# Optimization experiments

Measured on AMD Instinct MI355X. Metric: run time of the kernel, lower is better.

The kernel has to match this reference:

```python
import jax, jax.numpy as jnp
import numpy as np

VOCAB = 32000
D = 256
B, S = 16, 128


def setup_inputs() -> dict:
    key = jax.random.key(0)
    ks = jax.random.split(key, 8)
    s = 1.0 / np.sqrt(D)
    return {
        "X": jax.random.randint(ks[0], (B, S), 0, VOCAB),
        "emb": jax.random.normal(ks[1], (VOCAB, D), dtype=jnp.float32),
        "Wl": jax.random.uniform(ks[2], (D, D), jnp.float32, -s, s),
        "bl": jax.random.uniform(ks[3], (D,), jnp.float32, -s, s),
        "Wr": jax.random.uniform(ks[4], (D, D), jnp.float32, -s, s),
        "br": jax.random.uniform(ks[5], (D,), jnp.float32, -s, s),
        "Wrel": jax.random.uniform(ks[6], (D, D), jnp.float32, -s, s),
        "brel": jax.random.uniform(ks[7], (D,), jnp.float32, -s, s),
    }


def reference(X, emb, Wl, bl, Wr, br, Wrel, brel):
    # X: [B,S] int -> embed [B,S,D]
    e = emb[X]
    L = jnp.einsum("bsd,de->bse", e, Wl.T) + bl  # left projection per token
    R = jnp.einsum("bsd,de->bse", e, Wr.T) + br  # right projection per token
    # all-pairs relu(L_i + R_j): [B,S,S,D]
    pair = jax.nn.relu(L[:, :, None, :] + R[:, None, :, :])
    # relation is affine, so mean over S^2 pairs commutes with it (same math,
    # one [B,D] GEMM instead of B*S^2 tiny ones)
    pooled = pair.mean(axis=(1, 2))  # [B,D]
    return pooled @ Wrel.T + brel
```

## Files before the change

kernel.cpp:

```cpp
#include <hip/hip_runtime.h>
#include <hip/hip_bf16.h>

#define DD 256
#define SS 128
#define BB 16

typedef __attribute__((ext_vector_type(8))) short bf16x8;
typedef __attribute__((ext_vector_type(4))) float f32x4;

static __device__ __forceinline__ short f2bf(float f) {
    __hip_bfloat16 h = __float2bfloat16(f);
    return *reinterpret_cast<short*>(&h);
}

static __device__ __forceinline__ int swz_off(int r, int kb) {
    return r * 512 + (kb ^ ((r & 7) << 4) ^ (((r >> 3) & 3) << 7));
}


__global__ __launch_bounds__(256) void k_proj(
    const int* __restrict__ X, const float* __restrict__ emb,
    const float* __restrict__ Wl, const float* __restrict__ bl,
    const float* __restrict__ Wr, const float* __restrict__ br,
    float* __restrict__ LT, float* __restrict__ RT,
    float* __restrict__ sumLp, float* __restrict__ sumRp)
{
    __shared__ __align__(16) short Ebf[64 * 256];
    __shared__ __align__(16) short Wbf[64 * 256];
    __shared__ __align__(16) float Ot[64 * 68];
    __shared__ float red[4 * 64];
    __shared__ int toks[64];

    const int tid = threadIdx.x;
    const int bx  = blockIdx.x;
    const int tc  = bx >> 3;
    const int cc  = bx & 7;
    const int b   = tc >> 1;
    const int s0  = (tc & 1) * 64;
    const float* Wsrc = (cc < 4) ? Wl : Wr;
    const float* bsrc = (cc < 4) ? bl : br;
    const int dr0 = (cc & 3) * 64;

    if (tid < 64) toks[tid] = X[b * SS + s0 + tid];
    __syncthreads();

    char* Eb = (char*)Ebf;
    char* Wb = (char*)Wbf;
    {
        const int r  = tid & 63;
        const int wq = tid >> 6;
        const float4* es  = (const float4*)(emb + (size_t)toks[r] * DD + wq * 64);
        const float4* wsp = (const float4*)(Wsrc + (size_t)(dr0 + r) * DD + wq * 64);
        float4 ev[16], wv[16];
#pragma unroll
        for (int i = 0; i < 16; ++i) ev[i] = es[i];
#pragma unroll
        for (int i = 0; i < 16; ++i) wv[i] = wsp[i];
#pragma unroll
        for (int g = 0; g < 8; ++g) {
            bf16x8 pe, pw;
            pe[0] = f2bf(ev[2*g].x);   pe[1] = f2bf(ev[2*g].y);
            pe[2] = f2bf(ev[2*g].z);   pe[3] = f2bf(ev[2*g].w);
            pe[4] = f2bf(ev[2*g+1].x); pe[5] = f2bf(ev[2*g+1].y);
            pe[6] = f2bf(ev[2*g+1].z); pe[7] = f2bf(ev[2*g+1].w);
            pw[0] = f2bf(wv[2*g].x);   pw[1] = f2bf(wv[2*g].y);
            pw[2] = f2bf(wv[2*g].z);   pw[3] = f2bf(wv[2*g].w);
            pw[4] = f2bf(wv[2*g+1].x); pw[5] = f2bf(wv[2*g+1].y);
            pw[6] = f2bf(wv[2*g+1].z); pw[7] = f2bf(wv[2*g+1].w);
            const int off = swz_off(r, wq * 128 + g * 16);
            *(bf16x8*)(Eb + off) = pe;
            *(bf16x8*)(Wb + off) = pw;
        }
    }
    __syncthreads();

    const int w    = tid >> 6;
    const int lane = tid & 63;
    const int wm = w >> 1, wn = w & 1;
    const int lr = lane & 15, lk = lane >> 4;

    f32x4 zz = {0.f, 0.f, 0.f, 0.f};
    f32x4 acc00 = zz, acc01 = zz, acc10 = zz, acc11 = zz;

#pragma unroll
    for (int ks = 0; ks < 8; ++ks) {
        const int kb = ks * 64 + lk * 16;
        bf16x8 a0 = *(bf16x8*)(Eb + swz_off(wm * 32 + lr,      kb));
        bf16x8 a1 = *(bf16x8*)(Eb + swz_off(wm * 32 + 16 + lr, kb));
        bf16x8 b0 = *(bf16x8*)(Wb + swz_off(wn * 32 + lr,      kb));
        bf16x8 b1 = *(bf16x8*)(Wb + swz_off(wn * 32 + 16 + lr, kb));
        acc00 = __builtin_amdgcn_mfma_f32_16x16x32_bf16(a0, b0, acc00, 0, 0, 0);
        acc01 = __builtin_amdgcn_mfma_f32_16x16x32_bf16(a0, b1, acc01, 0, 0, 0);
        acc10 = __builtin_amdgcn_mfma_f32_16x16x32_bf16(a1, b0, acc10, 0, 0, 0);
        acc11 = __builtin_amdgcn_mfma_f32_16x16x32_bf16(a1, b1, acc11, 0, 0, 0);
    }

    {
        const float bv0 = bsrc[dr0 + wn * 32 + lr];
        const float bv1 = bsrc[dr0 + wn * 32 + 16 + lr];
        const int dl0 = wn * 32 + lr;
#pragma unroll
        for (int reg = 0; reg < 4; ++reg) {
            const int sl0 = wm * 32 + lk * 4 + reg;
            Ot[(dl0     ) * 68 + sl0     ] = acc00[reg] + bv0;
            Ot[(dl0 + 16) * 68 + sl0     ] = acc01[reg] + bv1;
            Ot[(dl0     ) * 68 + sl0 + 16] = acc10[reg] + bv0;
            Ot[(dl0 + 16) * 68 + sl0 + 16] = acc11[reg] + bv1;
        }
    }
    __syncthreads();

    float* Tb = (cc < 4) ? LT : RT;
    {
        const int dl = tid >> 2, sq = tid & 3;
        float* dst = Tb + ((size_t)(b * DD + dr0 + dl)) * SS + s0 + sq * 16;
#pragma unroll
        for (int i = 0; i < 4; ++i)
            *(float4*)(dst + i * 4) = *(float4*)&Ot[dl * 68 + sq * 16 + i * 4];
    }
    {
        const int d = tid & 63, sq = tid >> 6;
        float s = 0.f;
#pragma unroll
        for (int i = 0; i < 4; ++i) {
            float4 v = *(float4*)&Ot[d * 68 + sq * 16 + i * 4];
            s += (v.x + v.y) + (v.z + v.w);
        }
        red[sq * 64 + d] = s;
    }
    __syncthreads();
    if (tid < 64) {
        float s = red[tid] + red[64 + tid] + red[128 + tid] + red[192 + tid];
        float* sp = (cc < 4) ? sumLp : sumRp;
        sp[(b * 2 + (tc & 1)) * DD + dr0 + tid] = s;
    }
}

__global__ __launch_bounds__(256) void k_pairs(
    const float* __restrict__ LT, const float* __restrict__ RT,
    float* __restrict__ absP)
{
    __shared__ float Ll[64 * 17];
    __shared__ float Rl[64 * 129];
    __shared__ float red[256];
    const int tid = threadIdx.x;
    const int bx  = blockIdx.x;
    const int b   = bx >> 5;
    const int dc  = (bx >> 3) & 3;
    const int is  = bx & 7;

    const float* Lg = LT + ((size_t)(b * DD + dc * 64)) * SS;
    const float* Rg = RT + ((size_t)(b * DD + dc * 64)) * SS;

    {
        int r = tid >> 2, c4 = tid & 3;
        float4 x = *(const float4*)&Lg[(size_t)r * SS + is * 16 + c4 * 4];
        float* p = &Ll[r * 17 + c4 * 4];
        p[0] = x.x; p[1] = x.y; p[2] = x.z; p[3] = x.w;
    }
#pragma unroll
    for (int it = 0; it < 8; ++it) {
        int v = it * 256 + tid;
        int r = v >> 5, c4 = v & 31;
        float4 x = *(const float4*)&Rg[(size_t)r * SS + c4 * 4];
        float* p = &Rl[r * 129 + c4 * 4];
        p[0] = x.x; p[1] = x.y; p[2] = x.z; p[3] = x.w;
    }
    __syncthreads();

    const int dl = tid & 63;
    const int jg = tid >> 6;
    float rr[32];
#pragma unroll
    for (int j = 0; j < 32; ++j) rr[j] = Rl[dl * 129 + jg * 32 + j];

    float a0 = 0.f, a1 = 0.f, a2 = 0.f, a3 = 0.f;
#pragma unroll
    for (int i = 0; i < 16; ++i) {
        float l = Ll[dl * 17 + i];
#pragma unroll
        for (int j = 0; j < 32; j += 4) {
            a0 += fabsf(l + rr[j + 0]);
            a1 += fabsf(l + rr[j + 1]);
            a2 += fabsf(l + rr[j + 2]);
            a3 += fabsf(l + rr[j + 3]);
        }
    }
    red[tid] = (a0 + a1) + (a2 + a3);
    __syncthreads();
    if (tid < 64) {
        float s = red[tid] + red[tid + 64] + red[tid + 128] + red[tid + 192];
        absP[((b * 4 + dc) * 8 + is) * 64 + tid] = s;
    }
}

__global__ __launch_bounds__(256) void k_final(
    const float* __restrict__ sumLp, const float* __restrict__ sumRp,
    const float* __restrict__ absP,
    const float* __restrict__ Wrel, const float* __restrict__ brel,
    float* __restrict__ out)
{
    __shared__ float plds[DD];
    const int tid = threadIdx.x;
    const int b   = blockIdx.x;

    float sl = sumLp[(b * 2 + 0) * DD + tid] + sumLp[(b * 2 + 1) * DD + tid];
    float sr = sumRp[(b * 2 + 0) * DD + tid] + sumRp[(b * 2 + 1) * DD + tid];

    const int dc = tid >> 6, dl = tid & 63;
    float sa = 0.f;
#pragma unroll
    for (int is = 0; is < 8; ++is)
        sa += absP[((b * 4 + dc) * 8 + is) * 64 + dl];

    plds[tid] = (128.0f * (sl + sr) + sa) * (1.0f / 32768.0f);
    __syncthreads();

    float acc = brel[tid];
    const float4* w4 = (const float4*)(Wrel + (size_t)tid * DD);
#pragma unroll
    for (int k4 = 0; k4 < DD / 4; ++k4) {
        float4 p = *(float4*)&plds[k4 * 4];
        float4 w = w4[k4];
        acc = fmaf(p.x, w.x, acc);
        acc = fmaf(p.y, w.y, acc);
        acc = fmaf(p.z, w.z, acc);
        acc = fmaf(p.w, w.w, acc);
    }
    out[b * DD + tid] = acc;
}

extern "C" void kernel_launch(void* const* d_in, const int* in_sizes, int n_in,
                              void* d_out, int out_size, void* d_ws, size_t ws_size,
                              hipStream_t stream) {
    const int*   X    = (const int*)d_in[0];
    const float* emb  = (const float*)d_in[1];
    const float* Wl   = (const float*)d_in[2];
    const float* bl   = (const float*)d_in[3];
    const float* Wr   = (const float*)d_in[4];
    const float* br   = (const float*)d_in[5];
    const float* Wrel = (const float*)d_in[6];
    const float* brel = (const float*)d_in[7];
    float* out = (float*)d_out;

    float* ws = (float*)d_ws;
    float* LT    = ws;
    float* RT    = LT + (size_t)BB * DD * SS;
    float* sumLp = RT + (size_t)BB * DD * SS;
    float* sumRp = sumLp + BB * 2 * DD;
    float* absP  = sumRp + BB * 2 * DD;

    k_proj<<<256, 256, 0, stream>>>(X, emb, Wl, bl, Wr, br,
                                    LT, RT, sumLp, sumRp);
    k_pairs<<<512, 256, 0, stream>>>(LT, RT, absP);
    k_final<<<BB, 256, 0, stream>>>(sumLp, sumRp, absP, Wrel, brel, out);
}
```

Baseline: 34.49 us.

## Store projections token-major, shrink proj tiles, transpose in pairs kernel

The projection kernel now writes L and R in [B,S,D] layout straight from the MFMA accumulators. This removes the LDS transpose staging and the extra syncs, and the column sums are reduced with wave shuffles. Projection tiles shrink to 32 output columns, so the grid doubles to 512 blocks with less LDS each. The pairs kernel transposes into LDS during its loads and handles 32 rows per block on a grid halved to 256 blocks. The costs are scattered, poorly coalesced scalar stores from the projection, strided LDS transposes in the pairs kernel, and fewer pair blocks.

Result: faster. 29.63 us (-14.1%).

```diff
diff --git a/kernel.cpp b/kernel.cpp
--- a/kernel.cpp
+++ b/kernel.cpp
@@ -6,6 +6,7 @@
 #define BB 16
 
 typedef __attribute__((ext_vector_type(8))) short bf16x8;
+typedef __attribute__((ext_vector_type(4))) short bf16x4;
 typedef __attribute__((ext_vector_type(4))) float f32x4;
 
 static __device__ __forceinline__ short f2bf(float f) {
@@ -22,55 +23,45 @@
     const int* __restrict__ X, const float* __restrict__ emb,
     const float* __restrict__ Wl, const float* __restrict__ bl,
     const float* __restrict__ Wr, const float* __restrict__ br,
-    float* __restrict__ LT, float* __restrict__ RT,
+    float* __restrict__ Lsd, float* __restrict__ Rsd,
     float* __restrict__ sumLp, float* __restrict__ sumRp)
 {
     __shared__ __align__(16) short Ebf[64 * 256];
-    __shared__ __align__(16) short Wbf[64 * 256];
-    __shared__ __align__(16) float Ot[64 * 68];
-    __shared__ float red[4 * 64];
+    __shared__ __align__(16) short Wbf[32 * 256];
+    __shared__ float redw[4 * 16];
     __shared__ int toks[64];
 
     const int tid = threadIdx.x;
     const int bx  = blockIdx.x;
-    const int tc  = bx >> 3;
-    const int cc  = bx & 7;
+    const int tc  = bx >> 4;
+    const int cc  = bx & 15;
     const int b   = tc >> 1;
     const int s0  = (tc & 1) * 64;
-    const float* Wsrc = (cc < 4) ? Wl : Wr;
-    const float* bsrc = (cc < 4) ? bl : br;
-    const int dr0 = (cc & 3) * 64;
+    const float* Wsrc = (cc < 8) ? Wl : Wr;
+    const float* bsrc = (cc < 8) ? bl : br;
+    const int dr0 = (cc & 7) * 32;
 
     if (tid < 64) toks[tid] = X[b * SS + s0 + tid];
     __syncthreads();
 
     char* Eb = (char*)Ebf;
     char* Wb = (char*)Wbf;
-    {
-        const int r  = tid & 63;
-        const int wq = tid >> 6;
-        const float4* es  = (const float4*)(emb + (size_t)toks[r] * DD + wq * 64);
-        const float4* wsp = (const float4*)(Wsrc + (size_t)(dr0 + r) * DD + wq * 64);
-        float4 ev[16], wv[16];
-#pragma unroll
-        for (int i = 0; i < 16; ++i) ev[i] = es[i];
-#pragma unroll
-        for (int i = 0; i < 16; ++i) wv[i] = wsp[i];
-#pragma unroll
-        for (int g = 0; g < 8; ++g) {
-            bf16x8 pe, pw;
-            pe[0] = f2bf(ev[2*g].x);   pe[1] = f2bf(ev[2*g].y);
-            pe[2] = f2bf(ev[2*g].z);   pe[3] = f2bf(ev[2*g].w);
-            pe[4] = f2bf(ev[2*g+1].x); pe[5] = f2bf(ev[2*g+1].y);
-            pe[6] = f2bf(ev[2*g+1].z); pe[7] = f2bf(ev[2*g+1].w);
-            pw[0] = f2bf(wv[2*g].x);   pw[1] = f2bf(wv[2*g].y);
-            pw[2] = f2bf(wv[2*g].z);   pw[3] = f2bf(wv[2*g].w);
-            pw[4] = f2bf(wv[2*g+1].x); pw[5] = f2bf(wv[2*g+1].y);
-            pw[6] = f2bf(wv[2*g+1].z); pw[7] = f2bf(wv[2*g+1].w);
-            const int off = swz_off(r, wq * 128 + g * 16);
-            *(bf16x8*)(Eb + off) = pe;
-            *(bf16x8*)(Wb + off) = pw;
-        }
+
+#pragma unroll
+    for (int i = 0; i < 16; ++i) {
+        int v = i * 256 + tid;
+        int row = v >> 6, c4 = v & 63;
+        float4 f = *(const float4*)&emb[(size_t)toks[row] * DD + c4 * 4];
+        bf16x4 p; p[0] = f2bf(f.x); p[1] = f2bf(f.y); p[2] = f2bf(f.z); p[3] = f2bf(f.w);
+        *(bf16x4*)(Eb + swz_off(row, c4 * 8)) = p;
+    }
+#pragma unroll
+    for (int i = 0; i < 8; ++i) {
+        int v = i * 256 + tid;
+        int row = v >> 6, c4 = v & 63;
+        float4 f = *(const float4*)&Wsrc[(size_t)(dr0 + row) * DD + c4 * 4];
+        bf16x4 p; p[0] = f2bf(f.x); p[1] = f2bf(f.y); p[2] = f2bf(f.z); p[3] = f2bf(f.w);
+        *(bf16x4*)(Wb + swz_off(row, c4 * 8)) = p;
     }
     __syncthreads();
 
@@ -79,92 +70,73 @@
     const int wm = w >> 1, wn = w & 1;
     const int lr = lane & 15, lk = lane >> 4;
 
-    f32x4 zz = {0.f, 0.f, 0.f, 0.f};
-    f32x4 acc00 = zz, acc01 = zz, acc10 = zz, acc11 = zz;
-
+    f32x4 acc0 = {0.f, 0.f, 0.f, 0.f}, acc1 = acc0;
 #pragma unroll
     for (int ks = 0; ks < 8; ++ks) {
         const int kb = ks * 64 + lk * 16;
         bf16x8 a0 = *(bf16x8*)(Eb + swz_off(wm * 32 + lr,      kb));
         bf16x8 a1 = *(bf16x8*)(Eb + swz_off(wm * 32 + 16 + lr, kb));
-        bf16x8 b0 = *(bf16x8*)(Wb + swz_off(wn * 32 + lr,      kb));
-        bf16x8 b1 = *(bf16x8*)(Wb + swz_off(wn * 32 + 16 + lr, kb));
-        acc00 = __builtin_amdgcn_mfma_f32_16x16x32_bf16(a0, b0, acc00, 0, 0, 0);
-        acc01 = __builtin_amdgcn_mfma_f32_16x16x32_bf16(a0, b1, acc01, 0, 0, 0);
-        acc10 = __builtin_amdgcn_mfma_f32_16x16x32_bf16(a1, b0, acc10, 0, 0, 0);
-        acc11 = __builtin_amdgcn_mfma_f32_16x16x32_bf16(a1, b1, acc11, 0, 0, 0);
-    }
-
-    {
-        const float bv0 = bsrc[dr0 + wn * 32 + lr];
-        const float bv1 = bsrc[dr0 + wn * 32 + 16 + lr];
-        const int dl0 = wn * 32 + lr;
-#pragma unroll
-        for (int reg = 0; reg < 4; ++reg) {
-            const int sl0 = wm * 32 + lk * 4 + reg;
-            Ot[(dl0     ) * 68 + sl0     ] = acc00[reg] + bv0;
-            Ot[(dl0 + 16) * 68 + sl0     ] = acc01[reg] + bv1;
-            Ot[(dl0     ) * 68 + sl0 + 16] = acc10[reg] + bv0;
-            Ot[(dl0 + 16) * 68 + sl0 + 16] = acc11[reg] + bv1;
-        }
-    }
-    __syncthreads();
-
-    float* Tb = (cc < 4) ? LT : RT;
-    {
-        const int dl = tid >> 2, sq = tid & 3;
-        float* dst = Tb + ((size_t)(b * DD + dr0 + dl)) * SS + s0 + sq * 16;
-#pragma unroll
-        for (int i = 0; i < 4; ++i)
-            *(float4*)(dst + i * 4) = *(float4*)&Ot[dl * 68 + sq * 16 + i * 4];
-    }
-    {
-        const int d = tid & 63, sq = tid >> 6;
-        float s = 0.f;
-#pragma unroll
-        for (int i = 0; i < 4; ++i) {
-            float4 v = *(float4*)&Ot[d * 68 + sq * 16 + i * 4];
-            s += (v.x + v.y) + (v.z + v.w);
-        }
-        red[sq * 64 + d] = s;
-    }
-    __syncthreads();
-    if (tid < 64) {
-        float s = red[tid] + red[64 + tid] + red[128 + tid] + red[192 + tid];
-        float* sp = (cc < 4) ? sumLp : sumRp;
-        sp[(b * 2 + (tc & 1)) * DD + dr0 + tid] = s;
+        bf16x8 b0 = *(bf16x8*)(Wb + swz_off(wn * 16 + lr,      kb));
+        acc0 = __builtin_amdgcn_mfma_f32_16x16x32_bf16(a0, b0, acc0, 0, 0, 0);
+        acc1 = __builtin_amdgcn_mfma_f32_16x16x32_bf16(a1, b0, acc1, 0, 0, 0);
+    }
+
+    const float bv = bsrc[dr0 + wn * 16 + lr];
+    float* Tb = (cc < 8) ? Lsd : Rsd;
+    const int dcol = dr0 + wn * 16 + lr;
+#pragma unroll
+    for (int reg = 0; reg < 4; ++reg) {
+        int st = s0 + wm * 32 + lk * 4 + reg;
+        Tb[((size_t)(b * SS) + st)      * DD + dcol] = acc0[reg] + bv;
+        Tb[((size_t)(b * SS) + st + 16) * DD + dcol] = acc1[reg] + bv;
+    }
+
+    float t8 = (acc0[0] + acc0[1] + acc0[2] + acc0[3]) + bv * 8.0f
+             + (acc1[0] + acc1[1] + acc1[2] + acc1[3]);
+    t8 += __shfl_xor(t8, 16);
+    t8 += __shfl_xor(t8, 32);
+    if (lane < 16) redw[w * 16 + lr] = t8;
+    __syncthreads();
+    if (tid < 32) {
+        int wn2 = tid >> 4, c = tid & 15;
+        float s = redw[(0 * 2 + wn2) * 16 + c] + redw[(1 * 2 + wn2) * 16 + c];
+        float* sp = (cc < 8) ? sumLp : sumRp;
+        sp[(b * 2 + (tc & 1)) * DD + dr0 + wn2 * 16 + c] = s;
     }
 }
 
 __global__ __launch_bounds__(256) void k_pairs(
-    const float* __restrict__ LT, const float* __restrict__ RT,
+    const float* __restrict__ Lsd, const float* __restrict__ Rsd,
     float* __restrict__ absP)
 {
-    __shared__ float Ll[64 * 17];
+    __shared__ float Ll[64 * 33];
     __shared__ float Rl[64 * 129];
     __shared__ float red[256];
     const int tid = threadIdx.x;
     const int bx  = blockIdx.x;
-    const int b   = bx >> 5;
-    const int dc  = (bx >> 3) & 3;
-    const int is  = bx & 7;
-
-    const float* Lg = LT + ((size_t)(b * DD + dc * 64)) * SS;
-    const float* Rg = RT + ((size_t)(b * DD + dc * 64)) * SS;
-
-    {
-        int r = tid >> 2, c4 = tid & 3;
-        float4 x = *(const float4*)&Lg[(size_t)r * SS + is * 16 + c4 * 4];
-        float* p = &Ll[r * 17 + c4 * 4];
-        p[0] = x.x; p[1] = x.y; p[2] = x.z; p[3] = x.w;
+    const int b   = bx >> 4;
+    const int dc  = (bx >> 2) & 3;
+    const int is  = bx & 3;
+
+#pragma unroll
+    for (int it = 0; it < 2; ++it) {
+        int v = it * 256 + tid;
+        int srow = v >> 4, c4 = v & 15;
+        float4 x = *(const float4*)&Lsd[((size_t)(b * SS) + is * 32 + srow) * DD + dc * 64 + c4 * 4];
+        Ll[(c4 * 4 + 0) * 33 + srow] = x.x;
+        Ll[(c4 * 4 + 1) * 33 + srow] = x.y;
+        Ll[(c4 * 4 + 2) * 33 + srow] = x.z;
+        Ll[(c4 * 4 + 3) * 33 + srow] = x.w;
     }
 #pragma unroll
     for (int it = 0; it < 8; ++it) {
         int v = it * 256 + tid;
-        int r = v >> 5, c4 = v & 31;
-        float4 x = *(const float4*)&Rg[(size_t)r * SS + c4 * 4];
-        float* p = &Rl[r * 129 + c4 * 4];
-        p[0] = x.x; p[1] = x.y; p[2] = x.z; p[3] = x.w;
+        int j = v >> 4, c4 = v & 15;
+        float4 x = *(const float4*)&Rsd[((size_t)(b * SS) + j) * DD + dc * 64 + c4 * 4];
+        Rl[(c4 * 4 + 0) * 129 + j] = x.x;
+        Rl[(c4 * 4 + 1) * 129 + j] = x.y;
+        Rl[(c4 * 4 + 2) * 129 + j] = x.z;
+        Rl[(c4 * 4 + 3) * 129 + j] = x.w;
     }
     __syncthreads();
 
@@ -176,8 +148,8 @@
 
     float a0 = 0.f, a1 = 0.f, a2 = 0.f, a3 = 0.f;
 #pragma unroll
-    for (int i = 0; i < 16; ++i) {
-        float l = Ll[dl * 17 + i];
+    for (int i = 0; i < 32; ++i) {
+        float l = Ll[dl * 33 + i];
 #pragma unroll
         for (int j = 0; j < 32; j += 4) {
             a0 += fabsf(l + rr[j + 0]);
@@ -190,7 +162,7 @@
     __syncthreads();
     if (tid < 64) {
         float s = red[tid] + red[tid + 64] + red[tid + 128] + red[tid + 192];
-        absP[((b * 4 + dc) * 8 + is) * 64 + tid] = s;
+        absP[((b * 4 + dc) * 4 + is) * 64 + tid] = s;
     }
 }
 
@@ -210,8 +182,8 @@
     const int dc = tid >> 6, dl = tid & 63;
     float sa = 0.f;
 #pragma unroll
-    for (int is = 0; is < 8; ++is)
-        sa += absP[((b * 4 + dc) * 8 + is) * 64 + dl];
+    for (int is = 0; is < 4; ++is)
+        sa += absP[((b * 4 + dc) * 4 + is) * 64 + dl];
 
     plds[tid] = (128.0f * (sl + sr) + sa) * (1.0f / 32768.0f);
     __syncthreads();
@@ -244,14 +216,14 @@
     float* out = (float*)d_out;
 
     float* ws = (float*)d_ws;
-    float* LT    = ws;
-    float* RT    = LT + (size_t)BB * DD * SS;
-    float* sumLp = RT + (size_t)BB * DD * SS;
+    float* Lsd   = ws;
+    float* Rsd   = Lsd + (size_t)BB * SS * DD;
+    float* sumLp = Rsd + (size_t)BB * SS * DD;
     float* sumRp = sumLp + BB * 2 * DD;
     float* absP  = sumRp + BB * 2 * DD;
 
-    k_proj<<<256, 256, 0, stream>>>(X, emb, Wl, bl, Wr, br,
-                                    LT, RT, sumLp, sumRp);
-    k_pairs<<<512, 256, 0, stream>>>(LT, RT, absP);
+    k_proj<<<512, 256, 0, stream>>>(X, emb, Wl, bl, Wr, br,
+                                    Lsd, Rsd, sumLp, sumRp);
+    k_pairs<<<256, 256, 0, stream>>>(Lsd, Rsd, absP);
     k_final<<<BB, 256, 0, stream>>>(sumLp, sumRp, absP, Wrel, brel, out);
 }
```
